# Kernel optimization log

Measured on AMD Instinct MI355X. Metric: run time of the kernel, lower is better.

Reference implementation:

```python
import jax, jax.numpy as jnp
import numpy as np

B, C, H, W = 2, 4, 32, 256   # batch, num_classes (class 0 = background), range-image H x W
N = H * W                    # candidate points per (batch, class)
RADIUS = 3.0
KM_ITERS = 1
COORD_SCALE = 60.0           # spread lidar x/y so radius-3 NMS is non-trivial


def setup_inputs() -> dict:
    key = jax.random.key(0)
    k1, k2 = jax.random.split(key)
    segmented_channels = jax.random.normal(k1, (B, C, H, W), dtype=jnp.float32)
    lidar = jax.random.normal(k2, (B, 2, H, W), dtype=jnp.float32) * COORD_SCALE
    return {"segmented_channels": segmented_channels, "lidar": lidar}


def _radius_nms(points, mask, radius):
    # Greedy radius NMS in index order: keep point i iff no earlier kept point
    # lies within `radius`. Masked-out points are never kept (keep init = mask).
    n = points.shape[0]
    idx = jnp.arange(n)
    r2 = radius * radius

    def step(keep, i):
        d2 = jnp.sum((points - points[i]) ** 2, axis=-1)       # [N]
        suppress = keep & (d2 < r2) & (idx > i) & keep[i]
        return keep & ~suppress, None

    keep, _ = jax.lax.scan(step, mask, idx)
    return keep


def _kmeans(points, mask, keep, iters):
    # Centers initialized at the NMS-kept points (same index space as points).
    # Each valid class point is assigned to nearest valid center; centers move
    # to the mean of their assigned points.
    n = points.shape[0]
    centers = points
    w = mask.astype(points.dtype)
    BIG = jnp.asarray(1e30, points.dtype)
    for _ in range(iters):
        d2 = jnp.sum((points[:, None, :] - centers[None, :, :]) ** 2, axis=-1)  # [N,N]
        d2 = jnp.where(keep[None, :], d2, BIG)
        assign = jnp.argmin(d2, axis=1)                         # [N]
        sums = jax.ops.segment_sum(points * w[:, None], assign, num_segments=n)
        cnt = jax.ops.segment_sum(w, assign, num_segments=n)
        upd = sums / jnp.maximum(cnt, 1.0)[:, None]
        centers = jnp.where((keep & (cnt > 0))[:, None], upd, centers)
    return centers * keep[:, None].astype(points.dtype)


def reference(segmented_channels, lidar):
    ind = jnp.argmax(segmented_channels, axis=1)                # [B,H,W] class id per cell
    pts = jnp.stack([lidar[:, 0], lidar[:, 1]], axis=-1).reshape(B, N, 2)
    # boolean class masks for foreground classes 1..C-1
    cls_mask = jnp.stack([ind == c for c in range(1, C)], axis=1).reshape(B, C - 1, N)
    pts_all = jnp.broadcast_to(pts[:, None], (B, C - 1, N, 2)).reshape(B * (C - 1), N, 2)
    mask_all = cls_mask.reshape(B * (C - 1), N)

    def per_bc(args):
        p, m = args
        keep = _radius_nms(p, m, RADIUS)
        centers = _kmeans(p, m, keep, KM_ITERS)
        return centers, keep

    centers, keep = jax.lax.map(per_bc, (pts_all, mask_all))
    # centers: padded [B, C-1, N, 2]; keep marks which rows are real detections
    return centers.reshape(B, C - 1, N, 2), keep.reshape(B, C - 1, N)
```

## Files before the change

### kernel.cpp

```cpp
#include <hip/hip_runtime.h>

#define NPTS 8192
#define BCLS 4
#define NP   6
#define R2   9.0f
#define RAD  3.0f
#define GRD  64
#define NCELL (GRD*GRD)
#define LDSK 2048
#define OWNMAX 8

#define ST_U 0
#define ST_A 1
#define ST_D 2

__global__ __launch_bounds__(1024) void k_fused(
    const float* __restrict__ seg, const float* __restrict__ lidar,
    float* __restrict__ sumx, float* __restrict__ sumy, float* __restrict__ cntw,
    float* __restrict__ out)
{
    const int p = blockIdx.x;
    const int b = p / 3, cls = p % 3 + 1;
    const int tid = threadIdx.x, lane = tid & 63, wv = tid >> 6;
    const int base = p * NPTS;

    __shared__ float2 sp[NPTS];
    __shared__ unsigned short cidx[NPTS];
    __shared__ unsigned short sortid[NPTS];
    __shared__ unsigned int cellpack[NCELL];
    __shared__ unsigned char st[NPTS];
    __shared__ float ksx[LDSK], ksy[LDSK], kcn[LDSK];
    __shared__ unsigned long long ballots[128];
    __shared__ unsigned int base128[128];
    __shared__ unsigned int wtot[16];
    __shared__ float redbuf[4][16];
    __shared__ float sbminx, sbminy, scell;
    __shared__ int sM, sK;

    volatile unsigned char* vst = (volatile unsigned char*)st;
    float* ok = out + (size_t)2 * NP * NPTS + base;

    for (int k = tid; k < NPTS; k += 1024) { st[k] = ST_U; ok[k] = 0.f; }
    {
        float2* oc = (float2*)(out + (size_t)2 * base);
        for (int k = tid; k < NPTS; k += 1024) oc[k] = make_float2(0.f, 0.f);
    }
    for (int k = tid; k < NCELL; k += 1024) cellpack[k] = 0u;
    for (int k = tid; k < LDSK; k += 1024) { ksx[k] = 0.f; ksy[k] = 0.f; kcn[k] = 0.f; }

    const float* segb = seg + (size_t)b * BCLS * NPTS;
    const float* lx = lidar + (size_t)b * 2 * NPTS;
    const float* ly = lx + NPTS;
    for (int c0 = 0; c0 < 8; ++c0) {
        int n = c0 * 1024 + tid;
        float bv = segb[n];
        int bc = 0;
        #pragma unroll
        for (int c2 = 1; c2 < BCLS; ++c2) {
            float v = segb[c2 * NPTS + n];
            if (v > bv) { bv = v; bc = c2; }
        }
        unsigned long long bal = __ballot(bc == cls);
        if (lane == 0) ballots[c0 * 16 + wv] = bal;
    }
    __syncthreads();
    if (wv == 0) {
        unsigned int p0 = (unsigned int)__popcll(ballots[2 * lane]);
        unsigned int p1 = (unsigned int)__popcll(ballots[2 * lane + 1]);
        unsigned int s = p0 + p1, v = s;
        for (int d = 1; d < 64; d <<= 1) {
            unsigned int u = __shfl_up(v, d, 64);
            if (lane >= d) v += u;
        }
        base128[2 * lane] = v - s;
        base128[2 * lane + 1] = v - p1;
        if (lane == 63) sM = (int)v;
    }
    __syncthreads();
    const int M = sM;
    for (int c0 = 0; c0 < 8; ++c0) {
        unsigned long long bal = ballots[c0 * 16 + wv];
        if ((bal >> lane) & 1ull) {
            int n = c0 * 1024 + tid;
            int pos = (int)base128[c0 * 16 + wv] + __popcll(bal & ((1ull << lane) - 1ull));
            sp[pos] = make_float2(lx[n], ly[n]);
            cidx[pos] = (unsigned short)n;
        }
    }
    __syncthreads();

    {
        float mnx = 3e38f, mxx = -3e38f, mny = 3e38f, mxy = -3e38f;
        for (int i = tid; i < M; i += 1024) {
            float2 q = sp[i];
            mnx = fminf(mnx, q.x); mxx = fmaxf(mxx, q.x);
            mny = fminf(mny, q.y); mxy = fmaxf(mxy, q.y);
        }
        for (int d = 32; d; d >>= 1) {
            mnx = fminf(mnx, __shfl_xor(mnx, d, 64));
            mxx = fmaxf(mxx, __shfl_xor(mxx, d, 64));
            mny = fminf(mny, __shfl_xor(mny, d, 64));
            mxy = fmaxf(mxy, __shfl_xor(mxy, d, 64));
        }
        if (lane == 0) { redbuf[0][wv] = mnx; redbuf[1][wv] = mxx;
                         redbuf[2][wv] = mny; redbuf[3][wv] = mxy; }
    }
    __syncthreads();
    if (tid == 0) {
        float a = redbuf[0][0], b2 = redbuf[1][0], c = redbuf[2][0], d = redbuf[3][0];
        for (int q = 1; q < 16; ++q) {
            a = fminf(a, redbuf[0][q]); b2 = fmaxf(b2, redbuf[1][q]);
            c = fminf(c, redbuf[2][q]); d = fmaxf(d, redbuf[3][q]);
        }
        sbminx = a; sbminy = c;
        scell = fmaxf(2.0f * RAD, fmaxf(b2 - a, d - c) / 63.0f);
    }
    __syncthreads();
    const float bminx = sbminx, bminy = sbminy, inv = 1.0f / scell;

    for (int i = tid; i < M; i += 1024) {
        float2 q = sp[i];
        int ix = min(GRD - 1, max(0, (int)((q.x - bminx) * inv)));
        int iy = min(GRD - 1, max(0, (int)((q.y - bminy) * inv)));
        atomicAdd(&cellpack[iy * GRD + ix], 1u);
    }
    __syncthreads();
    {
        unsigned int c4[4], t4 = 0;
        #pragma unroll
        for (int q = 0; q < 4; ++q) { c4[q] = cellpack[tid * 4 + q]; t4 += c4[q]; }
        unsigned int v = t4;
        for (int d = 1; d < 64; d <<= 1) {
            unsigned int u = __shfl_up(v, d, 64);
            if (lane >= d) v += u;
        }
        if (lane == 63) wtot[wv] = v;
        __syncthreads();
        if (tid == 0) {
            unsigned int acc = 0;
            for (int q = 0; q < 16; ++q) { unsigned int t = wtot[q]; wtot[q] = acc; acc += t; }
        }
        __syncthreads();
        unsigned int excl = wtot[wv] + v - t4;
        #pragma unroll
        for (int q = 0; q < 4; ++q) { cellpack[tid * 4 + q] = excl << 16; excl += c4[q]; }
    }
    __syncthreads();
    for (int i = tid; i < M; i += 1024) {
        float2 q = sp[i];
        int ix = min(GRD - 1, max(0, (int)((q.x - bminx) * inv)));
        int iy = min(GRD - 1, max(0, (int)((q.y - bminy) * inv)));
        unsigned int old = atomicAdd(&cellpack[iy * GRD + ix], 1u);
        sortid[(old >> 16) + (old & 0xffffu)] = (unsigned short)i;
    }
    __syncthreads();

    #define ROW_FLAGS(CY, CX0, CX1, I, ME, DEAD, UNDEC)                           \
    {                                                                             \
        unsigned int wa = cellpack[(CY) * GRD + (CX0)];                           \
        unsigned int wb = cellpack[(CY) * GRD + (CX1)];                           \
        unsigned int e0 = wa >> 16, e1 = (wb >> 16) + (wb & 0xffffu);             \
        for (unsigned int e = e0; e < e1; ++e) {                                  \
            int j = sortid[e];                                                    \
            float2 q = sp[j];                                                     \
            unsigned char sv = vst[j];                                            \
            float dx = __fsub_rn(ME.x, q.x), dy = __fsub_rn(ME.y, q.y);           \
            float d2 = __fadd_rn(__fmul_rn(dx, dx), __fmul_rn(dy, dy));           \
            bool in = (d2 < R2) & (j < (I));                                      \
            DEAD  |= in & (sv == ST_A);                                           \
            UNDEC |= in & (sv == ST_U);                                           \
        }                                                                         \
    }
    #define SCAN_FLAGS(I, ME, DEAD, UNDEC)                                        \
    {                                                                             \
        int cx0 = max(0, (int)((ME.x - RAD - bminx) * inv));                      \
        int cx1 = min(GRD - 1, (int)((ME.x + RAD - bminx) * inv));                \
        int cy0 = max(0, (int)((ME.y - RAD - bminy) * inv));                      \
        int cy1 = min(GRD - 1, (int)((ME.y + RAD - bminy) * inv));                \
        DEAD = false; UNDEC = false;                                              \
        ROW_FLAGS(cy0, cx0, cx1, I, ME, DEAD, UNDEC);                             \
        if (cy1 > cy0) ROW_FLAGS(cy1, cx0, cx1, I, ME, DEAD, UNDEC);              \
    }

    {
        int own[OWNMAX];
        float2 ops[OWNMAX];
        int nown = 0;
        for (int g = tid; g < M; g += 1024) {
            int i = sortid[g];
            own[nown] = i;
            ops[nown] = sp[i];
            ++nown;
        }
        int nres = 0;
        for (int spin = 0; nres < nown && spin < (1 << 17); ++spin) {
            for (int k = 0; k < nown; ++k) {
                int i = own[k];
                if (i < 0) continue;
                float2 me = ops[k];
                bool dead, undec;
                SCAN_FLAGS(i, me, dead, undec);
                if (dead)       { st[i] = ST_D; own[k] = -1; ++nres; }
                else if (!undec){ st[i] = ST_A; own[k] = -1; ++nres; }
            }
        }
    }
    for (;;) {
        bool any = false;
        for (int i = tid; i < M; i += 1024) {
            if (st[i] != ST_U) continue;
            float2 me = sp[i];
            bool dead, undec;
            SCAN_FLAGS(i, me, dead, undec);
            if (dead) st[i] = ST_D;
            else if (!undec) st[i] = ST_A;
            else any = true;
        }
        if (__syncthreads_count(any) == 0) break;
    }

    for (int k = 0; k < 8; ++k) {
        int i = (k << 10) + tid;
        unsigned long long bal = __ballot(st[i] == ST_A);
        if (lane == 0) ballots[(k << 4) + wv] = bal;
    }
    __syncthreads();
    if (wv == 0) {
        unsigned int p0 = (unsigned int)__popcll(ballots[2 * lane]);
        unsigned int p1 = (unsigned int)__popcll(ballots[2 * lane + 1]);
        unsigned int s = p0 + p1, v = s;
        for (int d = 1; d < 64; d <<= 1) {
            unsigned int u = __shfl_up(v, d, 64);
            if (lane >= d) v += u;
        }
        base128[2 * lane] = v - s;
        base128[2 * lane + 1] = v - p1;
        if (lane == 63) sK = (int)v;
    }
    __syncthreads();
    #define KRANK(J) ((int)base128[(J) >> 6] +                                    \
                      __popcll(ballots[(J) >> 6] & ((1ull << ((J) & 63)) - 1ull)))
    if (sK > LDSK) {
        for (int k = tid; k < NPTS; k += 1024) {
            sumx[base + k] = 0.f; sumy[base + k] = 0.f; cntw[base + k] = 0.f;
        }
        __syncthreads();
    }

    #define ROW_ARGMIN(CY, CX0, CX1, ME, BD, BJ)                                  \
    {                                                                             \
        unsigned int wa = cellpack[(CY) * GRD + (CX0)];                           \
        unsigned int wb = cellpack[(CY) * GRD + (CX1)];                           \
        unsigned int e0 = wa >> 16, e1 = (wb >> 16) + (wb & 0xffffu);             \
        for (unsigned int e = e0; e < e1; ++e) {                                  \
            int j = sortid[e];                                                    \
            float2 q = sp[j];                                                     \
            unsigned char sv = st[j];                                             \
            float dx = __fsub_rn(ME.x, q.x), dy = __fsub_rn(ME.y, q.y);           \
            float d2 = __fadd_rn(__fmul_rn(dx, dx), __fmul_rn(dy, dy));           \
            bool better = (sv == ST_A) & ((d2 < BD) | ((d2 == BD) & (j < BJ)));   \
            BD = better ? d2 : BD;                                                \
            BJ = better ? j : BJ;                                                 \
        }                                                                         \
    }
    for (int g = tid; g < M; g += 1024) {
        int i = sortid[g];
        float2 me = sp[i];
        int bj;
        if (st[i] == ST_A) {
            bj = i;
        } else {
            int cx0 = max(0, (int)((me.x - RAD - bminx) * inv));
            int cx1 = min(GRD - 1, (int)((me.x + RAD - bminx) * inv));
            int cy0 = max(0, (int)((me.y - RAD - bminy) * inv));
            int cy1 = min(GRD - 1, (int)((me.y + RAD - bminy) * inv));
            float bd = 3e38f;
            bj = -1;
            ROW_ARGMIN(cy0, cx0, cx1, me, bd, bj);
            if (cy1 > cy0) ROW_ARGMIN(cy1, cx0, cx1, me, bd, bj);
            if (bj < 0) continue;
        }
        int r = KRANK(bj);
        if (r < LDSK) {
            atomicAdd(&ksx[r], me.x);
            atomicAdd(&ksy[r], me.y);
            atomicAdd(&kcn[r], 1.0f);
        } else {
            atomicAdd(&sumx[base + bj], me.x);
            atomicAdd(&sumy[base + bj], me.y);
            atomicAdd(&cntw[base + bj], 1.0f);
        }
    }
    __syncthreads();

    for (int i = tid; i < M; i += 1024) {
        if (st[i] != ST_A) continue;
        int n = cidx[i];
        int r = KRANK(i);
        float sx, sy, c;
        if (r < LDSK) { sx = ksx[r]; sy = ksy[r]; c = kcn[r]; }
        else { sx = sumx[base + i]; sy = sumy[base + i]; c = cntw[base + i]; }
        out[2 * (base + n)]     = sx / c;
        out[2 * (base + n) + 1] = sy / c;
        ok[n] = 1.0f;
    }
}

extern "C" void kernel_launch(void* const* d_in, const int* in_sizes, int n_in,
                              void* d_out, int out_size, void* d_ws, size_t ws_size,
                              hipStream_t stream) {
    const float* seg   = (const float*)d_in[0];
    const float* lidar = (const float*)d_in[1];
    float* out = (float*)d_out;

    const size_t A = (size_t)NP * NPTS;
    float* sumx = (float*)d_ws;
    float* sumy = sumx + A;
    float* cntw = sumy + A;

    k_fused<<<NP, 1024, 0, stream>>>(seg, lidar, sumx, sumy, cntw, out);
}
```

Measured before the change: 123.1 us.

## Store points in cell-sorted order and resolve NMS with per-thread DFS

Points are now scattered directly into cell-sorted order, with the original index and NMS state packed into one word per point. This removes the compaction pass and the sortid indirection during neighbour scans. The spin-loop NMS resolver is replaced by a per-thread depth-first walk that follows the first undecided earlier neighbour and uses a small LDS stack. The walk is meant to cut repeated rescans of unresolved points, at the cost of more divergent control flow and a fallback chain walk when the stack overflows.

```diff
diff --git a/kernel.cpp b/kernel.cpp
--- a/kernel.cpp
+++ b/kernel.cpp
@@ -8,11 +8,10 @@
 #define GRD  64
 #define NCELL (GRD*GRD)
 #define LDSK 2048
-#define OWNMAX 8
-
-#define ST_U 0
-#define ST_A 1
-#define ST_D 2
+
+#define ST_U 0u
+#define ST_A 1u
+#define ST_D 2u
 
 __global__ __launch_bounds__(1024) void k_fused(
     const float* __restrict__ seg, const float* __restrict__ lidar,
@@ -24,11 +23,10 @@
     const int tid = threadIdx.x, lane = tid & 63, wv = tid >> 6;
     const int base = p * NPTS;
 
-    __shared__ float2 sp[NPTS];
-    __shared__ unsigned short cidx[NPTS];
-    __shared__ unsigned short sortid[NPTS];
+    __shared__ float2 sps[NPTS];
+    __shared__ unsigned int cmb[NPTS];
     __shared__ unsigned int cellpack[NCELL];
-    __shared__ unsigned char st[NPTS];
+    __shared__ unsigned short stk[8][1024];
     __shared__ float ksx[LDSK], ksy[LDSK], kcn[LDSK];
     __shared__ unsigned long long ballots[128];
     __shared__ unsigned int base128[128];
@@ -37,10 +35,10 @@
     __shared__ float sbminx, sbminy, scell;
     __shared__ int sM, sK;
 
-    volatile unsigned char* vst = (volatile unsigned char*)st;
+    volatile unsigned int* vcmb = (volatile unsigned int*)cmb;
     float* ok = out + (size_t)2 * NP * NPTS + base;
 
-    for (int k = tid; k < NPTS; k += 1024) { st[k] = ST_U; ok[k] = 0.f; }
+    for (int k = tid; k < NPTS; k += 1024) { cmb[k] = ST_U; ok[k] = 0.f; }
     {
         float2* oc = (float2*)(out + (size_t)2 * base);
         for (int k = tid; k < NPTS; k += 1024) oc[k] = make_float2(0.f, 0.f);
@@ -63,38 +61,27 @@
         unsigned long long bal = __ballot(bc == cls);
         if (lane == 0) ballots[c0 * 16 + wv] = bal;
     }
+    for (int n = tid; n < NPTS; n += 1024) sps[n] = make_float2(lx[n], ly[n]);
     __syncthreads();
     if (wv == 0) {
-        unsigned int p0 = (unsigned int)__popcll(ballots[2 * lane]);
-        unsigned int p1 = (unsigned int)__popcll(ballots[2 * lane + 1]);
-        unsigned int s = p0 + p1, v = s;
-        for (int d = 1; d < 64; d <<= 1) {
-            unsigned int u = __shfl_up(v, d, 64);
-            if (lane >= d) v += u;
-        }
-        base128[2 * lane] = v - s;
-        base128[2 * lane + 1] = v - p1;
-        if (lane == 63) sM = (int)v;
-    }
-    __syncthreads();
-    const int M = sM;
-    for (int c0 = 0; c0 < 8; ++c0) {
-        unsigned long long bal = ballots[c0 * 16 + wv];
-        if ((bal >> lane) & 1ull) {
-            int n = c0 * 1024 + tid;
-            int pos = (int)base128[c0 * 16 + wv] + __popcll(bal & ((1ull << lane) - 1ull));
-            sp[pos] = make_float2(lx[n], ly[n]);
-            cidx[pos] = (unsigned short)n;
-        }
-    }
-    __syncthreads();
-
+        unsigned int s = (unsigned int)__popcll(ballots[2 * lane]) +
+                         (unsigned int)__popcll(ballots[2 * lane + 1]);
+        for (int d = 1; d < 64; d <<= 1) s += __shfl_xor(s, d, 64);
+        if (lane == 0) sM = (int)s;
+    }
+
+    const unsigned long long mw = ballots[tid >> 3];
     {
         float mnx = 3e38f, mxx = -3e38f, mny = 3e38f, mxy = -3e38f;
-        for (int i = tid; i < M; i += 1024) {
-            float2 q = sp[i];
-            mnx = fminf(mnx, q.x); mxx = fmaxf(mxx, q.x);
-            mny = fminf(mny, q.y); mxy = fmaxf(mxy, q.y);
+        #pragma unroll
+        for (int q = 0; q < 8; ++q) {
+            int n = tid * 8 + q;
+            bool m = (mw >> (((tid & 7) << 3) + q)) & 1ull;
+            float2 c = sps[n];
+            if (m) {
+                mnx = fminf(mnx, c.x); mxx = fmaxf(mxx, c.x);
+                mny = fminf(mny, c.y); mxy = fmaxf(mxy, c.y);
+            }
         }
         for (int d = 32; d; d >>= 1) {
             mnx = fminf(mnx, __shfl_xor(mnx, d, 64));
@@ -117,12 +104,20 @@
     }
     __syncthreads();
     const float bminx = sbminx, bminy = sbminy, inv = 1.0f / scell;
-
-    for (int i = tid; i < M; i += 1024) {
-        float2 q = sp[i];
-        int ix = min(GRD - 1, max(0, (int)((q.x - bminx) * inv)));
-        int iy = min(GRD - 1, max(0, (int)((q.y - bminy) * inv)));
-        atomicAdd(&cellpack[iy * GRD + ix], 1u);
+    const int M = sM;
+
+    float xq[8], yq[8];
+    int cellq[8];
+    #pragma unroll
+    for (int q = 0; q < 8; ++q) {
+        int n = tid * 8 + q;
+        bool m = (mw >> (((tid & 7) << 3) + q)) & 1ull;
+        float2 c = sps[n];
+        xq[q] = c.x; yq[q] = c.y;
+        int ix = min(GRD - 1, max(0, (int)((c.x - bminx) * inv)));
+        int iy = min(GRD - 1, max(0, (int)((c.y - bminy) * inv)));
+        cellq[q] = m ? (iy * GRD + ix) : -1;
+        if (m) atomicAdd(&cellpack[iy * GRD + ix], 1u);
     }
     __syncthreads();
     {
@@ -146,82 +141,93 @@
         for (int q = 0; q < 4; ++q) { cellpack[tid * 4 + q] = excl << 16; excl += c4[q]; }
     }
     __syncthreads();
-    for (int i = tid; i < M; i += 1024) {
-        float2 q = sp[i];
-        int ix = min(GRD - 1, max(0, (int)((q.x - bminx) * inv)));
-        int iy = min(GRD - 1, max(0, (int)((q.y - bminy) * inv)));
-        unsigned int old = atomicAdd(&cellpack[iy * GRD + ix], 1u);
-        sortid[(old >> 16) + (old & 0xffffu)] = (unsigned short)i;
-    }
-    __syncthreads();
-
-    #define ROW_FLAGS(CY, CX0, CX1, I, ME, DEAD, UNDEC)                           \
+    #pragma unroll
+    for (int q = 0; q < 8; ++q) {
+        if (cellq[q] >= 0) {
+            unsigned int old = atomicAdd(&cellpack[cellq[q]], 1u);
+            unsigned int pos = (old >> 16) + (old & 0xffffu);
+            sps[pos] = make_float2(xq[q], yq[q]);
+            cmb[pos] = ((unsigned int)(tid * 8 + q) << 2) | ST_U;
+        }
+    }
+    __syncthreads();
+
+    #define ROW_DFS(CY, CX0, CX1, NI, ME, DEAD, FU)                               \
     {                                                                             \
         unsigned int wa = cellpack[(CY) * GRD + (CX0)];                           \
         unsigned int wb = cellpack[(CY) * GRD + (CX1)];                           \
-        unsigned int e0 = wa >> 16, e1 = (wb >> 16) + (wb & 0xffffu);             \
-        for (unsigned int e = e0; e < e1; ++e) {                                  \
-            int j = sortid[e];                                                    \
-            float2 q = sp[j];                                                     \
-            unsigned char sv = vst[j];                                            \
-            float dx = __fsub_rn(ME.x, q.x), dy = __fsub_rn(ME.y, q.y);           \
+        unsigned int f0 = wa >> 16, f1 = (wb >> 16) + (wb & 0xffffu);             \
+        for (unsigned int f = f0; f < f1; ++f) {                                  \
+            unsigned int wf = vcmb[f];                                            \
+            float2 q = sps[f];                                                    \
+            float dx = __fsub_rn((ME).x, q.x), dy = __fsub_rn((ME).y, q.y);       \
             float d2 = __fadd_rn(__fmul_rn(dx, dx), __fmul_rn(dy, dy));           \
-            bool in = (d2 < R2) & (j < (I));                                      \
-            DEAD  |= in & (sv == ST_A);                                           \
-            UNDEC |= in & (sv == ST_U);                                           \
+            bool in = (d2 < R2) & ((int)(wf >> 2) < (NI));                        \
+            DEAD |= in & ((wf & 3u) == ST_A);                                     \
+            if (in & ((wf & 3u) == ST_U) & ((FU) < 0)) FU = (int)f;               \
         }                                                                         \
     }
-    #define SCAN_FLAGS(I, ME, DEAD, UNDEC)                                        \
+    #define SCAN_DFS(NI, ME, DEAD, FU)                                            \
     {                                                                             \
-        int cx0 = max(0, (int)((ME.x - RAD - bminx) * inv));                      \
-        int cx1 = min(GRD - 1, (int)((ME.x + RAD - bminx) * inv));                \
-        int cy0 = max(0, (int)((ME.y - RAD - bminy) * inv));                      \
-        int cy1 = min(GRD - 1, (int)((ME.y + RAD - bminy) * inv));                \
-        DEAD = false; UNDEC = false;                                              \
-        ROW_FLAGS(cy0, cx0, cx1, I, ME, DEAD, UNDEC);                             \
-        if (cy1 > cy0) ROW_FLAGS(cy1, cx0, cx1, I, ME, DEAD, UNDEC);              \
-    }
-
-    {
-        int own[OWNMAX];
-        float2 ops[OWNMAX];
-        int nown = 0;
-        for (int g = tid; g < M; g += 1024) {
-            int i = sortid[g];
-            own[nown] = i;
-            ops[nown] = sp[i];
-            ++nown;
-        }
-        int nres = 0;
-        for (int spin = 0; nres < nown && spin < (1 << 17); ++spin) {
-            for (int k = 0; k < nown; ++k) {
-                int i = own[k];
-                if (i < 0) continue;
-                float2 me = ops[k];
-                bool dead, undec;
-                SCAN_FLAGS(i, me, dead, undec);
-                if (dead)       { st[i] = ST_D; own[k] = -1; ++nres; }
-                else if (!undec){ st[i] = ST_A; own[k] = -1; ++nres; }
+        int cx0 = max(0, (int)(((ME).x - RAD - bminx) * inv));                    \
+        int cx1 = min(GRD - 1, (int)(((ME).x + RAD - bminx) * inv));              \
+        int cy0 = max(0, (int)(((ME).y - RAD - bminy) * inv));                    \
+        int cy1 = min(GRD - 1, (int)(((ME).y + RAD - bminy) * inv));              \
+        DEAD = false; FU = -1;                                                    \
+        ROW_DFS(cy0, cx0, cx1, NI, ME, DEAD, FU);                                 \
+        if (cy1 > cy0) ROW_DFS(cy1, cx0, cx1, NI, ME, DEAD, FU);                  \
+    }
+
+    for (int e0 = tid; e0 < M; e0 += 1024) {
+        if ((vcmb[e0] & 3u) != ST_U) continue;
+        int top = 0;
+        stk[0][tid] = (unsigned short)e0;
+        while (top >= 0) {
+            int e = stk[top][tid];
+            unsigned int w = vcmb[e];
+            if ((w & 3u) != ST_U) { --top; continue; }
+            int ni = (int)(w >> 2);
+            float2 me = sps[e];
+            bool dead; int fu;
+            SCAN_DFS(ni, me, dead, fu);
+            if (dead)        { cmb[e] = ((unsigned int)ni << 2) | ST_D; --top; }
+            else if (fu < 0) { cmb[e] = ((unsigned int)ni << 2) | ST_A; --top; }
+            else if (top < 7)  stk[++top][tid] = (unsigned short)fu;
+            else {
+                int ec = fu;
+                for (;;) {
+                    unsigned int wc = vcmb[ec];
+                    if ((wc & 3u) != ST_U) break;
+                    int nc = (int)(wc >> 2);
+                    float2 mc = sps[ec];
+                    bool dd; int fc;
+                    SCAN_DFS(nc, mc, dd, fc);
+                    if (dd)        { cmb[ec] = ((unsigned int)nc << 2) | ST_D; break; }
+                    else if (fc < 0){ cmb[ec] = ((unsigned int)nc << 2) | ST_A; break; }
+                    ec = fc;
+                }
             }
         }
     }
     for (;;) {
         bool any = false;
-        for (int i = tid; i < M; i += 1024) {
-            if (st[i] != ST_U) continue;
-            float2 me = sp[i];
-            bool dead, undec;
-            SCAN_FLAGS(i, me, dead, undec);
-            if (dead) st[i] = ST_D;
-            else if (!undec) st[i] = ST_A;
+        for (int e = tid; e < M; e += 1024) {
+            unsigned int w = cmb[e];
+            if ((w & 3u) != ST_U) continue;
+            int ni = (int)(w >> 2);
+            float2 me = sps[e];
+            bool dead; int fu;
+            SCAN_DFS(ni, me, dead, fu);
+            if (dead)        cmb[e] = ((unsigned int)ni << 2) | ST_D;
+            else if (fu < 0) cmb[e] = ((unsigned int)ni << 2) | ST_A;
             else any = true;
         }
         if (__syncthreads_count(any) == 0) break;
     }
 
     for (int k = 0; k < 8; ++k) {
-        int i = (k << 10) + tid;
-        unsigned long long bal = __ballot(st[i] == ST_A);
+        int e = (k << 10) + tid;
+        unsigned long long bal = __ballot((cmb[e] & 3u) == ST_A);
         if (lane == 0) ballots[(k << 4) + wv] = bal;
     }
     __syncthreads();
@@ -238,8 +244,8 @@
         if (lane == 63) sK = (int)v;
     }
     __syncthreads();
-    #define KRANK(J) ((int)base128[(J) >> 6] +                                    \
-                      __popcll(ballots[(J) >> 6] & ((1ull << ((J) & 63)) - 1ull)))
+    #define KRANK(E) ((int)base128[(E) >> 6] +                                    \
+                      __popcll(ballots[(E) >> 6] & ((1ull << ((E) & 63)) - 1ull)))
     if (sK > LDSK) {
         for (int k = tid; k < NPTS; k += 1024) {
             sumx[base + k] = 0.f; sumy[base + k] = 0.f; cntw[base + k] = 0.f;
@@ -247,59 +253,63 @@
         __syncthreads();
     }
 
-    #define ROW_ARGMIN(CY, CX0, CX1, ME, BD, BJ)                                  \
+    #define ROW_ARGMIN(CY, CX0, CX1, ME, BD, BE, BN)                              \
     {                                                                             \
         unsigned int wa = cellpack[(CY) * GRD + (CX0)];                           \
         unsigned int wb = cellpack[(CY) * GRD + (CX1)];                           \
-        unsigned int e0 = wa >> 16, e1 = (wb >> 16) + (wb & 0xffffu);             \
-        for (unsigned int e = e0; e < e1; ++e) {                                  \
-            int j = sortid[e];                                                    \
-            float2 q = sp[j];                                                     \
-            unsigned char sv = st[j];                                             \
-            float dx = __fsub_rn(ME.x, q.x), dy = __fsub_rn(ME.y, q.y);           \
+        unsigned int f0 = wa >> 16, f1 = (wb >> 16) + (wb & 0xffffu);             \
+        for (unsigned int f = f0; f < f1; ++f) {                                  \
+            unsigned int wf = cmb[f];                                             \
+            float2 q = sps[f];                                                    \
+            float dx = __fsub_rn((ME).x, q.x), dy = __fsub_rn((ME).y, q.y);       \
             float d2 = __fadd_rn(__fmul_rn(dx, dx), __fmul_rn(dy, dy));           \
-            bool better = (sv == ST_A) & ((d2 < BD) | ((d2 == BD) & (j < BJ)));   \
+            int nf = (int)(wf >> 2);                                              \
+            bool better = ((wf & 3u) == ST_A) &                                   \
+                          ((d2 < BD) | ((d2 == BD) & (nf < BN)));                 \
             BD = better ? d2 : BD;                                                \
-            BJ = better ? j : BJ;                                                 \
+            BE = better ? (int)f : BE;                                            \
+            BN = better ? nf : BN;                                                \
         }                                                                         \
     }
-    for (int g = tid; g < M; g += 1024) {
-        int i = sortid[g];
-        float2 me = sp[i];
-        int bj;
-        if (st[i] == ST_A) {
-            bj = i;
+    for (int e = tid; e < M; e += 1024) {
+        unsigned int w = cmb[e];
+        float2 me = sps[e];
+        int be;
+        if ((w & 3u) == ST_A) {
+            be = e;
         } else {
             int cx0 = max(0, (int)((me.x - RAD - bminx) * inv));
             int cx1 = min(GRD - 1, (int)((me.x + RAD - bminx) * inv));
             int cy0 = max(0, (int)((me.y - RAD - bminy) * inv));
             int cy1 = min(GRD - 1, (int)((me.y + RAD - bminy) * inv));
             float bd = 3e38f;
-            bj = -1;
-            ROW_ARGMIN(cy0, cx0, cx1, me, bd, bj);
-            if (cy1 > cy0) ROW_ARGMIN(cy1, cx0, cx1, me, bd, bj);
-            if (bj < 0) continue;
-        }
-        int r = KRANK(bj);
+            be = -1;
+            int bn = 1 << 30;
+            ROW_ARGMIN(cy0, cx0, cx1, me, bd, be, bn);
+            if (cy1 > cy0) ROW_ARGMIN(cy1, cx0, cx1, me, bd, be, bn);
+            if (be < 0) continue;
+        }
+        int r = KRANK(be);
         if (r < LDSK) {
             atomicAdd(&ksx[r], me.x);
             atomicAdd(&ksy[r], me.y);
             atomicAdd(&kcn[r], 1.0f);
         } else {
-            atomicAdd(&sumx[base + bj], me.x);
-            atomicAdd(&sumy[base + bj], me.y);
-            atomicAdd(&cntw[base + bj], 1.0f);
-        }
-    }
-    __syncthreads();
-
-    for (int i = tid; i < M; i += 1024) {
-        if (st[i] != ST_A) continue;
-        int n = cidx[i];
-        int r = KRANK(i);
+            atomicAdd(&sumx[base + be], me.x);
+            atomicAdd(&sumy[base + be], me.y);
+            atomicAdd(&cntw[base + be], 1.0f);
+        }
+    }
+    __syncthreads();
+
+    for (int e = tid; e < M; e += 1024) {
+        unsigned int w = cmb[e];
+        if ((w & 3u) != ST_A) continue;
+        int n = (int)(w >> 2);
+        int r = KRANK(e);
         float sx, sy, c;
         if (r < LDSK) { sx = ksx[r]; sy = ksy[r]; c = kcn[r]; }
-        else { sx = sumx[base + i]; sy = sumy[base + i]; c = cntw[base + i]; }
+        else { sx = sumx[base + e]; sy = sumy[base + e]; c = cntw[base + e]; }
         out[2 * (base + n)]     = sx / c;
         out[2 * (base + n) + 1] = sy / c;
         ok[n] = 1.0f;
```

Result: no change. 121.3 us (-1.4%).
